# Kernel tuning notes

Measured on AMD Instinct MI355X. Metric: run time of the kernel, lower is better.

The kernel has to match this reference:

```python
import jax, jax.numpy as jnp
import numpy as np

B, N = 1, 768
C_S, C_Z, C_H, H, PQ, PV = 384, 128, 16, 12, 4, 8
INF, EPS = 1e5, 1e-8
SOFTPLUS_INV_1 = 0.541324854612918


def _quat_to_rot(q):
    # q: [..., 4] unit quaternions (w, x, y, z) -> [..., 3, 3]
    w, x, y, z = q[..., 0], q[..., 1], q[..., 2], q[..., 3]
    R = jnp.stack([
        1 - 2 * (y * y + z * z), 2 * (x * y - w * z), 2 * (x * z + w * y),
        2 * (x * y + w * z), 1 - 2 * (x * x + z * z), 2 * (y * z - w * x),
        2 * (x * z - w * y), 2 * (y * z + w * x), 1 - 2 * (x * x + y * y),
    ], axis=-1)
    return R.reshape(q.shape[:-1] + (3, 3))


def setup_inputs() -> dict:
    key = jax.random.key(0)
    ks = jax.random.split(key, 24)
    def lin(k, din, dout):
        return jax.random.normal(k, (din, dout), jnp.float32) / np.sqrt(din)
    quat = jax.random.normal(ks[2], (B, N, 4), jnp.float32)
    quat = quat / jnp.linalg.norm(quat, axis=-1, keepdims=True)
    return {
        "s": jax.random.normal(ks[0], (B, N, C_S), jnp.float32),
        "z": jax.random.normal(ks[1], (B, N, N, C_Z), jnp.float32),
        "rot": _quat_to_rot(quat),
        "trans": 10.0 * jax.random.normal(ks[3], (B, N, 3), jnp.float32),
        "mask": jnp.ones((B, N), jnp.float32),
        "wq": lin(ks[4], C_S, H * C_H), "bq": jnp.zeros((H * C_H,), jnp.float32),
        "wkv": lin(ks[5], C_S, 2 * H * C_H), "bkv": jnp.zeros((2 * H * C_H,), jnp.float32),
        "wqp": lin(ks[6], C_S, H * PQ * 3), "bqp": jnp.zeros((H * PQ * 3,), jnp.float32),
        "wkvp": lin(ks[7], C_S, H * (PQ + PV) * 3), "bkvp": jnp.zeros((H * (PQ + PV) * 3,), jnp.float32),
        "wb": lin(ks[8], C_Z, H), "bb": jnp.zeros((H,), jnp.float32),
        "wdz": lin(ks[9], C_Z, C_Z // 4), "bdz": jnp.zeros((C_Z // 4,), jnp.float32),
        "head_weights": jnp.full((H,), SOFTPLUS_INV_1, jnp.float32),
        "wout": lin(ks[10], H * (C_Z // 4 + C_H + PV * 4), C_S),
        "bout": jnp.zeros((C_S,), jnp.float32),
    }


def reference(s, z, rot, trans, mask, wq, bq, wkv, bkv, wqp, bqp, wkvp, bkvp,
              wb, bb, wdz, bdz, head_weights, wout, bout):
    # scalar q, k, v: [B, N, H, C_H]
    q = (s @ wq + bq).reshape(B, N, H, C_H)
    kv = (s @ wkv + bkv).reshape(B, N, H, 2 * C_H)
    k, v = kv[..., :C_H], kv[..., C_H:]

    def make_pts(w, b, npts):
        p = s @ w + b                                       # [B, N, H*npts*3]
        p = jnp.stack(jnp.split(p, 3, axis=-1), axis=-1)    # [B, N, H*npts, 3]
        p = jnp.einsum('bnxy,bnpy->bnpx', rot, p) + trans[:, :, None, :]
        return p.reshape(B, N, H, npts, 3)

    q_pts = make_pts(wqp, bqp, PQ)                          # [B, N, H, PQ, 3]
    kv_pts = make_pts(wkvp, bkvp, PQ + PV)
    k_pts, v_pts = kv_pts[..., :PQ, :], kv_pts[..., PQ:, :]

    b_bias = z @ wb + bb                                    # [B, N, N, H]
    a = jnp.einsum('bihc,bjhc->bhij', q, k) * np.sqrt(1.0 / (3 * C_H))
    a = a + np.sqrt(1.0 / 3) * jnp.transpose(b_bias, (0, 3, 1, 2))

    disp = q_pts[:, :, None] - k_pts[:, None]               # [B, i, j, H, PQ, 3]
    pt_att = jnp.sum(disp ** 2, axis=-1)                    # [B, i, j, H, PQ]
    hw = jax.nn.softplus(head_weights) * np.sqrt(1.0 / (3 * (PQ * 9.0 / 2)))
    pt_att = -0.5 * jnp.sum(pt_att * hw[:, None], axis=-1)  # [B, i, j, H]
    a = a + jnp.transpose(pt_att, (0, 3, 1, 2))

    sq_mask = INF * (mask[:, :, None] * mask[:, None, :] - 1.0)
    a = jax.nn.softmax(a + sq_mask[:, None], axis=-1)       # [B, H, i, j]

    o = jnp.einsum('bhij,bjhc->bihc', a, v).reshape(B, N, -1)
    o_pt = jnp.einsum('bhij,bjhpx->bihpx', a, v_pts)        # [B, N, H, PV, 3]
    o_pt = jnp.einsum('bixy,bihpx->bihpy', rot, o_pt - trans[:, :, None, None, :])
    o_pt_norm = jnp.sqrt(jnp.sum(o_pt ** 2, axis=-1) + EPS).reshape(B, N, -1)
    o_pt = o_pt.reshape(B, N, -1, 3)

    pair_z = z @ wdz + bdz                                  # [B, N, N, C_Z//4]
    o_pair = jnp.einsum('bhij,bijc->bihc', a, pair_z).reshape(B, N, -1)

    feats = jnp.concatenate(
        [o, o_pt[..., 0], o_pt[..., 1], o_pt[..., 2], o_pt_norm, o_pair], axis=-1)
    return feats @ wout + bout
```

## Files before the change

kernel.cpp:

```cpp
#include <hip/hip_runtime.h>
#include <hip/hip_bf16.h>
#include <math.h>

#define NTOK 768
#define CS   384
#define CZ   128
#define NH   12
#define INF_ 100000.0f
#define EPS_ 1e-8f

typedef unsigned int  uint32;
typedef __attribute__((ext_vector_type(8))) short bf16x8;
typedef __attribute__((ext_vector_type(4))) float f32x4;

__device__ __forceinline__ uint32 bf16rn(float x) {
    uint32 u = __float_as_uint(x);
    return (u + 0x7fffu + ((u >> 16) & 1u)) >> 16;
}
__device__ __forceinline__ float bflo(uint32 u) { return __uint_as_float((u & 0xffffu) << 16); }
__device__ __forceinline__ float bfhi(uint32 u) { return __uint_as_float(u & 0xffff0000u); }
__device__ __forceinline__ uint32 pkbf(float a, float b) {
    union { unsigned short s[2]; uint32 u; } r;
    __hip_bfloat16 ha = __float2bfloat16(a);
    __hip_bfloat16 hb = __float2bfloat16(b);
    __builtin_memcpy(&r.s[0], &ha, 2);
    __builtin_memcpy(&r.s[1], &hb, 2);
    return r.u;
}

#define QK_SCALE 0.14433756729740643f
#define B_SCALE  0.5773502691896258f
#define HW_SCALE 0.13608276348795434f

__global__ __launch_bounds__(256) void k1a_gemm(
    const float* __restrict__ s,
    const float* __restrict__ wq, const float* __restrict__ wkv,
    const float* __restrict__ wqp, const float* __restrict__ wkvp,
    float* __restrict__ RAW)
{
    __shared__ float sA[32][72];
    __shared__ float sB[32][72];
    const int tid  = threadIdx.x;
    const int tok0 = blockIdx.x * 64;
    const int col0 = blockIdx.y * 64;

    const int m0 = (tid & 15) * 4;
    const int n0 = (tid >> 4) * 4;

    float4 acc[4];
    #pragma unroll
    for (int nn = 0; nn < 4; nn++) acc[nn] = make_float4(0.f, 0.f, 0.f, 0.f);

    const int lam = tid >> 2, lak = (tid & 3) * 8;
    const int lbk = tid >> 3, lbc = (tid & 7) * 8;
    const int gcol = col0 + lbc;
    const float* wsrc; int wwidth, woff;
    if (gcol < 192)      { wsrc = wq;   wwidth = 192; woff = gcol; }
    else if (gcol < 576) { wsrc = wkv;  wwidth = 384; woff = gcol - 192; }
    else if (gcol < 720) { wsrc = wqp;  wwidth = 144; woff = gcol - 576; }
    else                 { wsrc = wkvp; wwidth = 432; woff = gcol - 720; }

    for (int kb = 0; kb < CS; kb += 32) {
        const float4 a0 = *(const float4*)&s[(tok0 + lam) * CS + kb + lak];
        const float4 a1 = *(const float4*)&s[(tok0 + lam) * CS + kb + lak + 4];
        const float4 b0 = *(const float4*)&wsrc[(size_t)(kb + lbk) * wwidth + woff];
        const float4 b1 = *(const float4*)&wsrc[(size_t)(kb + lbk) * wwidth + woff + 4];
        __syncthreads();
        sA[lak + 0][lam] = a0.x; sA[lak + 1][lam] = a0.y;
        sA[lak + 2][lam] = a0.z; sA[lak + 3][lam] = a0.w;
        sA[lak + 4][lam] = a1.x; sA[lak + 5][lam] = a1.y;
        sA[lak + 6][lam] = a1.z; sA[lak + 7][lam] = a1.w;
        *(float4*)&sB[lbk][lbc]     = b0;
        *(float4*)&sB[lbk][lbc + 4] = b1;
        __syncthreads();
        #pragma unroll
        for (int k = 0; k < 32; k++) {
            const float4 av = *(const float4*)&sA[k][m0];
            const float4 bv = *(const float4*)&sB[k][n0];
            acc[0].x += av.x * bv.x; acc[0].y += av.y * bv.x; acc[0].z += av.z * bv.x; acc[0].w += av.w * bv.x;
            acc[1].x += av.x * bv.y; acc[1].y += av.y * bv.y; acc[1].z += av.z * bv.y; acc[1].w += av.w * bv.y;
            acc[2].x += av.x * bv.z; acc[2].y += av.y * bv.z; acc[2].z += av.z * bv.z; acc[2].w += av.w * bv.z;
            acc[3].x += av.x * bv.w; acc[3].y += av.y * bv.w; acc[3].z += av.z * bv.w; acc[3].w += av.w * bv.w;
        }
    }
    #pragma unroll
    for (int nn = 0; nn < 4; nn++)
        *(float4*)&RAW[(size_t)(col0 + n0 + nn) * NTOK + tok0 + m0] = acc[nn];
}

__global__ __launch_bounds__(256) void k1b_finish(
    const float* __restrict__ RAW,
    const float* __restrict__ rot, const float* __restrict__ trans,
    const float* __restrict__ bq, const float* __restrict__ bkv,
    const float* __restrict__ bqp, const float* __restrict__ bkvp,
    const float* __restrict__ head_weights,
    float* __restrict__ VT, float* __restrict__ QP, float* __restrict__ VPT,
    float* __restrict__ AP, float* __restrict__ BP,
    float* __restrict__ RQN, float* __restrict__ CKN)
{
    __shared__ float hwS[NH];
    const int tid = threadIdx.x;
    const int t  = blockIdx.x * 16 + (tid & 15);
    const int wk = tid >> 4;

    if (tid < NH) hwS[tid] = logf(1.0f + expf(head_weights[tid])) * HW_SCALE;

    float R[9], T3[3];
    #pragma unroll
    for (int x = 0; x < 9; x++) R[x] = rot[t * 9 + x];
    #pragma unroll
    for (int x = 0; x < 3; x++) T3[x] = trans[t * 3 + x];
    __syncthreads();

    for (int col = wk; col < 192; col += 16) {
        const int h = col >> 4, c = col & 15;
        AP[(size_t)(h * 28 + c) * NTOK + t] = QK_SCALE * (RAW[(size_t)col * NTOK + t] + bq[col]);
    }
    for (int idx = wk; idx < 192; idx += 16) {
        const int h = idx >> 4, c = idx & 15;
        BP[(size_t)(h * 28 + c) * NTOK + t] = RAW[(size_t)(192 + h * 32 + c) * NTOK + t] + bkv[h * 32 + c];
        VT[idx * NTOK + t] = RAW[(size_t)(192 + h * 32 + 16 + c) * NTOK + t] + bkv[h * 32 + 16 + c];
    }
    for (int pidx = wk; pidx < 48; pidx += 16) {
        const int h = pidx >> 2, p = pidx & 3;
        const float r0 = RAW[(size_t)(576 + 0 * 48 + pidx) * NTOK + t] + bqp[0 * 48 + pidx];
        const float r1 = RAW[(size_t)(576 + 1 * 48 + pidx) * NTOK + t] + bqp[1 * 48 + pidx];
        const float r2 = RAW[(size_t)(576 + 2 * 48 + pidx) * NTOK + t] + bqp[2 * 48 + pidx];
        #pragma unroll
        for (int x = 0; x < 3; x++) {
            const float v = R[x*3+0]*r0 + R[x*3+1]*r1 + R[x*3+2]*r2 + T3[x];
            QP[t * 144 + pidx * 3 + x] = v;
            AP[(size_t)(h * 28 + 16 + p * 3 + x) * NTOK + t] = hwS[h] * v;
        }
    }
    for (int pidx = wk; pidx < 144; pidx += 16) {
        const int h = pidx / 12, pp = pidx % 12;
        const float r0 = RAW[(size_t)(720 + 0 * 144 + pidx) * NTOK + t] + bkvp[0 * 144 + pidx];
        const float r1 = RAW[(size_t)(720 + 1 * 144 + pidx) * NTOK + t] + bkvp[1 * 144 + pidx];
        const float r2 = RAW[(size_t)(720 + 2 * 144 + pidx) * NTOK + t] + bkvp[2 * 144 + pidx];
        #pragma unroll
        for (int x = 0; x < 3; x++) {
            const float v = R[x*3+0]*r0 + R[x*3+1]*r1 + R[x*3+2]*r2 + T3[x];
            if (pp < 4) BP[(size_t)(h * 28 + 16 + pp * 3 + x) * NTOK + t] = v;
            else        VPT[((h * 8 + pp - 4) * 3 + x) * NTOK + t] = v;
        }
    }
    __syncthreads();
    if (wk < NH) {
        const int h = wk;
        float sq = 0.f, sk = 0.f;
        #pragma unroll
        for (int d = 0; d < 12; d++) {
            const float a = QP[t * 144 + h * 12 + d];
            sq += a * a;
            const float b = BP[(size_t)(h * 28 + 16 + d) * NTOK + t];
            sk += b * b;
        }
        RQN[h * NTOK + t] = -0.5f * hwS[h] * sq;
        CKN[h * NTOK + t] = -0.5f * hwS[h] * sk;
    }
}

__global__ __launch_bounds__(256) void k2_zproj_mfma(
    const float* __restrict__ z, const float* __restrict__ wb, const float* __restrict__ bb,
    const float* __restrict__ wdz, const float* __restrict__ bdz,
    float* __restrict__ BBT, uint32* __restrict__ PZB)
{
    __shared__ __align__(16) unsigned short wB[48 * 136];
    __shared__ float outS[2][64][52];
    __shared__ float bbS[12], bdzS[32];

    const int tid = threadIdx.x;
    const int i   = blockIdx.x;
    const int l   = tid & 63;
    const int jt  = tid >> 6;

    for (int idx = tid; idx < 48 * 64; idx += 256) {
        const int o = idx >> 6, k2 = (idx & 63) * 2;
        float f0, f1;
        if (o < 12)      { f0 = wb[k2 * 12 + o];         f1 = wb[(k2 + 1) * 12 + o]; }
        else if (o < 44) { f0 = wdz[k2 * 32 + (o - 12)]; f1 = wdz[(k2 + 1) * 32 + (o - 12)]; }
        else             { f0 = 0.f; f1 = 0.f; }
        *(uint32*)&wB[o * 136 + k2] = pkbf(f0, f1);
    }
    if (tid < 12) bbS[tid] = bb[tid];
    else if (tid >= 32 && tid < 64) bdzS[tid - 32] = bdz[tid - 32];
    __syncthreads();

    bf16x8 Bf[3][4];
    #pragma unroll
    for (int t = 0; t < 3; t++)
        #pragma unroll
        for (int ks = 0; ks < 4; ks++)
            Bf[t][ks] = *(const bf16x8*)&wB[(t * 16 + (l & 15)) * 136 + ks * 32 + (l >> 4) * 8];

    const float* zb = z + ((size_t)i * NTOK + jt * 16 + (l & 15)) * CZ + (l >> 4) * 8;

    float4 pa[8];
    #pragma unroll
    for (int ks = 0; ks < 4; ks++) {
        pa[2 * ks]     = *(const float4*)&zb[ks * 32];
        pa[2 * ks + 1] = *(const float4*)&zb[ks * 32 + 4];
    }

    for (int tile = 0; tile < 12; tile++) {
        const int j0  = tile * 64;
        const int buf = tile & 1;

        union { uint32 u[4]; bf16x8 v; } Au[4];
        #pragma unroll
        for (int ks = 0; ks < 4; ks++) {
            Au[ks].u[0] = pkbf(pa[2 * ks].x,     pa[2 * ks].y);
            Au[ks].u[1] = pkbf(pa[2 * ks].z,     pa[2 * ks].w);
            Au[ks].u[2] = pkbf(pa[2 * ks + 1].x, pa[2 * ks + 1].y);
            Au[ks].u[3] = pkbf(pa[2 * ks + 1].z, pa[2 * ks + 1].w);
        }
        if (tile < 11) {
            const float* zn = zb + (size_t)(tile + 1) * 64 * CZ;
            #pragma unroll
            for (int ks = 0; ks < 4; ks++) {
                pa[2 * ks]     = *(const float4*)&zn[ks * 32];
                pa[2 * ks + 1] = *(const float4*)&zn[ks * 32 + 4];
            }
        }

        f32x4 acc[3];
        #pragma unroll
        for (int t = 0; t < 3; t++) acc[t] = (f32x4){0.f, 0.f, 0.f, 0.f};
        #pragma unroll
        for (int ks = 0; ks < 4; ks++)
            #pragma unroll
            for (int t = 0; t < 3; t++)
                acc[t] = __builtin_amdgcn_mfma_f32_16x16x32_bf16(Au[ks].v, Bf[t][ks], acc[t], 0, 0, 0);

        #pragma unroll
        for (int t = 0; t < 3; t++) {
            const int o = t * 16 + (l & 15);
            #pragma unroll
            for (int v = 0; v < 4; v++)
                outS[buf][jt * 16 + (l >> 4) * 4 + v][o] = acc[t][v];
        }
        __syncthreads();

        for (int idx = tid; idx < 12 * 64; idx += 256) {
            const int o = idx >> 6, jl = idx & 63;
            BBT[((size_t)i * 12 + o) * NTOK + j0 + jl] = outS[buf][jl][o] + bbS[o];
        }
        for (int idx = tid; idx < 32 * 32; idx += 256) {
            const int c = idx >> 5, jp = idx & 31;
            const float f0 = outS[buf][jp * 2][12 + c] + bdzS[c];
            const float f1 = outS[buf][jp * 2 + 1][12 + c] + bdzS[c];
            PZB[(size_t)(i * 32 + c) * 384 + (j0 >> 1) + jp] = pkbf(f0, f1);
        }
    }
}

__global__ __launch_bounds__(256) void k3a_logits(
    const float* __restrict__ AP, const float* __restrict__ BP,
    const float* __restrict__ RQN, const float* __restrict__ CKN,
    const float* __restrict__ BBT, const float* __restrict__ mask,
    float* __restrict__ LG)
{
    __shared__ float sA[28][64];
    __shared__ float sB[28][64];
    const int tid = threadIdx.x;
    const int j0 = blockIdx.x * 64;
    const int i0 = blockIdx.y * 64;
    const int h  = blockIdx.z;

    #pragma unroll
    for (int t = 0; t < 7; t++) {
        const int idx = tid + t * 256;
        const int row = idx >> 6, col = idx & 63;
        sA[row][col] = AP[(size_t)(h * 28 + row) * NTOK + i0 + col];
        sB[row][col] = BP[(size_t)(h * 28 + row) * NTOK + j0 + col];
    }
    __syncthreads();

    const int m0 = (tid & 15) * 4;
    const int n0 = (tid >> 4) * 4;

    float4 acc[4];
    #pragma unroll
    for (int mm = 0; mm < 4; mm++) acc[mm] = make_float4(0.f, 0.f, 0.f, 0.f);

    #pragma unroll
    for (int k = 0; k < 28; k++) {
        const float4 av = *(const float4*)&sA[k][m0];
        const float4 bv = *(const float4*)&sB[k][n0];
        acc[0].x += av.x * bv.x; acc[0].y += av.x * bv.y; acc[0].z += av.x * bv.z; acc[0].w += av.x * bv.w;
        acc[1].x += av.y * bv.x; acc[1].y += av.y * bv.y; acc[1].z += av.y * bv.z; acc[1].w += av.y * bv.w;
        acc[2].x += av.z * bv.x; acc[2].y += av.z * bv.y; acc[2].z += av.z * bv.z; acc[2].w += av.z * bv.w;
        acc[3].x += av.w * bv.x; acc[3].y += av.w * bv.y; acc[3].z += av.w * bv.z; acc[3].w += av.w * bv.w;
    }

    const float4 ck = *(const float4*)&CKN[h * NTOK + j0 + n0];
    const float4 mj = *(const float4*)&mask[j0 + n0];
    #pragma unroll
    for (int mm = 0; mm < 4; mm++) {
        const int gi = i0 + m0 + mm;
        const float rq = RQN[h * NTOK + gi];
        const float mi = mask[gi];
        const float4 bb = *(const float4*)&BBT[((size_t)gi * NH + h) * NTOK + j0 + n0];
        float4 o;
        o.x = acc[mm].x + B_SCALE * bb.x + rq + ck.x + INF_ * (mi * mj.x - 1.0f);
        o.y = acc[mm].y + B_SCALE * bb.y + rq + ck.y + INF_ * (mi * mj.y - 1.0f);
        o.z = acc[mm].z + B_SCALE * bb.z + rq + ck.z + INF_ * (mi * mj.z - 1.0f);
        o.w = acc[mm].w + B_SCALE * bb.w + rq + ck.w + INF_ * (mi * mj.w - 1.0f);
        *(float4*)&LG[((size_t)gi * NH + h) * NTOK + j0 + n0] = o;
    }
}

__global__ __launch_bounds__(768) void k3b_attn(
    const float* __restrict__ LG,
    const float* __restrict__ VT, const float* __restrict__ VPT,
    const uint32* __restrict__ PZB,
    float* __restrict__ O, float* __restrict__ OPT, float* __restrict__ OPAIR)
{
    __shared__ float LB[NH][NTOK];
    const int i = blockIdx.x, tid = threadIdx.x;

    #pragma unroll
    for (int hh = 0; hh < NH; hh++)
        LB[hh][tid] = LG[((size_t)i * NH + hh) * NTOK + tid];
    __syncthreads();

    const int h = tid >> 6, l = tid & 63;

    {
        float m = -3.0e38f;
        for (int jj = l; jj < NTOK; jj += 64) m = fmaxf(m, LB[h][jj]);
        #pragma unroll
        for (int off = 32; off >= 1; off >>= 1) m = fmaxf(m, __shfl_xor(m, off));
        float ssum = 0.0f;
        for (int jj = l; jj < NTOK; jj += 64) {
            const float e = __expf(LB[h][jj] - m);
            LB[h][jj] = e;
            ssum += e;
        }
        #pragma unroll
        for (int off = 32; off >= 1; off >>= 1) ssum += __shfl_xor(ssum, off);
        const float inv = 1.0f / ssum;
        for (int jj = l; jj < NTOK; jj += 64) LB[h][jj] *= inv;
    }
    __syncthreads();

    #pragma unroll 2
    for (int r = 0; r < 40; r++) {
        const float4* src = (r < 16) ? (const float4*)&VT[(h * 16 + r) * NTOK]
                                     : (const float4*)&VPT[(h * 24 + (r - 16)) * NTOK];
        const float4 v0 = src[l],       p0 = *(const float4*)&LB[h][l * 4];
        const float4 v1 = src[64 + l],  p1 = *(const float4*)&LB[h][256 + l * 4];
        const float4 v2 = src[128 + l], p2 = *(const float4*)&LB[h][512 + l * 4];
        float acc = p0.x*v0.x + p0.y*v0.y + p0.z*v0.z + p0.w*v0.w
                  + p1.x*v1.x + p1.y*v1.y + p1.z*v1.z + p1.w*v1.w
                  + p2.x*v2.x + p2.y*v2.y + p2.z*v2.z + p2.w*v2.w;
        #pragma unroll
        for (int off = 32; off >= 1; off >>= 1) acc += __shfl_xor(acc, off);
        if (l == 0) {
            if (r < 16) O[i * 192 + h * 16 + r] = acc;
            else        OPT[i * 288 + h * 24 + (r - 16)] = acc;
        }
    }
    #pragma unroll 2
    for (int c = 0; c < 32; c++) {
        const uint2* src = (const uint2*)PZB + (size_t)(i * 32 + c) * 192;
        float a = 0.f;
        #pragma unroll
        for (int it = 0; it < 3; it++) {
            const uint2 u = src[it * 64 + l];
            const float4 p = *(const float4*)&LB[h][it * 256 + l * 4];
            a += p.x * bflo(u.x) + p.y * bfhi(u.x)
               + p.z * bflo(u.y) + p.w * bfhi(u.y);
        }
        #pragma unroll
        for (int off = 32; off >= 1; off >>= 1) a += __shfl_xor(a, off);
        if (l == 0) OPAIR[i * 384 + h * 32 + c] = a;
    }
}

#define K4T 8
__global__ __launch_bounds__(256) void k4_out(
    const float* __restrict__ O, const float* __restrict__ OPT, const float* __restrict__ OPAIR,
    const float* __restrict__ rot, const float* __restrict__ trans,
    const float* __restrict__ wout, const float* __restrict__ bout,
    float* __restrict__ out)
{
    __shared__ float f[K4T][960];
    const int n0 = blockIdx.x * K4T, tid = threadIdx.x;

    for (int idx = tid; idx < K4T * 192; idx += 256) {
        const int t = idx / 192, k = idx % 192;
        f[t][k] = O[(n0 + t) * 192 + k];
    }
    for (int idx = tid; idx < K4T * 384; idx += 256) {
        const int t = idx / 384, k = idx % 384;
        f[t][576 + k] = OPAIR[(n0 + t) * 384 + k];
    }
    for (int idx = tid; idx < K4T * 96; idx += 256) {
        const int t = idx / 96, hp = idx % 96;
        const int n = n0 + t;
        const float vx = OPT[n * 288 + hp * 3 + 0] - trans[n * 3 + 0];
        const float vy = OPT[n * 288 + hp * 3 + 1] - trans[n * 3 + 1];
        const float vz = OPT[n * 288 + hp * 3 + 2] - trans[n * 3 + 2];
        const float o0 = rot[n*9+0]*vx + rot[n*9+3]*vy + rot[n*9+6]*vz;
        const float o1 = rot[n*9+1]*vx + rot[n*9+4]*vy + rot[n*9+7]*vz;
        const float o2 = rot[n*9+2]*vx + rot[n*9+5]*vy + rot[n*9+8]*vz;
        f[t][192 + hp] = o0;
        f[t][288 + hp] = o1;
        f[t][384 + hp] = o2;
        f[t][480 + hp] = sqrtf(o0*o0 + o1*o1 + o2*o2 + EPS_);
    }
    __syncthreads();

    for (int o = tid; o < 384; o += 256) {
        float acc[K4T];
        #pragma unroll
        for (int t = 0; t < K4T; t++) acc[t] = bout[o];
        for (int kq = 0; kq < 240; kq++) {
            float4 fv[K4T];
            #pragma unroll
            for (int t = 0; t < K4T; t++) fv[t] = *(const float4*)&f[t][kq * 4];
            #pragma unroll
            for (int kk = 0; kk < 4; kk++) {
                const float wv = wout[(kq * 4 + kk) * 384 + o];
                #pragma unroll
                for (int t = 0; t < K4T; t++) {
                    const float fe = (kk == 0) ? fv[t].x : (kk == 1) ? fv[t].y
                                   : (kk == 2) ? fv[t].z : fv[t].w;
                    acc[t] += fe * wv;
                }
            }
        }
        #pragma unroll
        for (int t = 0; t < K4T; t++) out[(n0 + t) * 384 + o] = acc[t];
    }
}

extern "C" void kernel_launch(void* const* d_in, const int* in_sizes, int n_in,
                              void* d_out, int out_size, void* d_ws, size_t ws_size,
                              hipStream_t stream) {
    (void)in_sizes; (void)n_in; (void)out_size; (void)ws_size;
    const float* s     = (const float*)d_in[0];
    const float* z     = (const float*)d_in[1];
    const float* rot   = (const float*)d_in[2];
    const float* trans = (const float*)d_in[3];
    const float* mask  = (const float*)d_in[4];
    const float* wq    = (const float*)d_in[5];
    const float* bq    = (const float*)d_in[6];
    const float* wkv   = (const float*)d_in[7];
    const float* bkv   = (const float*)d_in[8];
    const float* wqp   = (const float*)d_in[9];
    const float* bqp   = (const float*)d_in[10];
    const float* wkvp  = (const float*)d_in[11];
    const float* bkvp  = (const float*)d_in[12];
    const float* wb    = (const float*)d_in[13];
    const float* bb    = (const float*)d_in[14];
    const float* wdz   = (const float*)d_in[15];
    const float* bdz   = (const float*)d_in[16];
    const float* hwts  = (const float*)d_in[17];
    const float* wout  = (const float*)d_in[18];
    const float* bout  = (const float*)d_in[19];
    float* out = (float*)d_out;

    float* ws = (float*)d_ws;
    float* Q     = ws;
    float* KT    = Q     + 147456;
    float* VT    = KT    + 147456;
    float* QP    = VT    + 147456;
    float* KPT   = QP    + 110592;
    float* VPT   = KPT   + 110592;
    float* O     = VPT   + 221184;
    float* OPT   = O     + 147456;
    float* OPAIR = OPT   + 221184;
    float* BBT   = OPAIR + 294912;
    uint32* PZB  = (uint32*)(BBT + 7077888);
    float* AP    = BBT + 7077888 + 9437184;
    float* BP    = AP  + 258048;
    float* RQN   = BP  + 258048;
    float* CKN   = RQN + 9216;
    float* LG    = CKN + 9216;
    float* RAW = BBT;

    hipLaunchKernelGGL(k1a_gemm, dim3(NTOK / 64, 1152 / 64), dim3(256), 0, stream,
                       s, wq, wkv, wqp, wkvp, RAW);
    hipLaunchKernelGGL(k1b_finish, dim3(NTOK / 16), dim3(256), 0, stream,
                       RAW, rot, trans, bq, bkv, bqp, bkvp, hwts,
                       VT, QP, VPT, AP, BP, RQN, CKN);
    hipLaunchKernelGGL(k2_zproj_mfma, dim3(NTOK), dim3(256), 0, stream,
                       z, wb, bb, wdz, bdz, BBT, PZB);
    hipLaunchKernelGGL(k3a_logits, dim3(NTOK / 64, NTOK / 64, NH), dim3(256), 0, stream,
                       AP, BP, RQN, CKN, BBT, mask, LG);
    hipLaunchKernelGGL(k3b_attn, dim3(NTOK), dim3(768), 0, stream,
                       LG, VT, VPT, PZB, O, OPT, OPAIR);
    hipLaunchKernelGGL(k4_out, dim3(NTOK / K4T), dim3(256), 0, stream,
                       O, OPT, OPAIR, rot, trans, wout, bout, out);
}
```

Baseline: 391.4 us.

## Fuse logits computation with softmax and attention, keeping probabilities in registers

Merges the separate logits kernel and attention kernel into one kernel per query row. Each wavefront computes its head's logits directly from the point-projection factors, keeps the softmax probabilities in registers, and drops the LG intermediate buffer and its global round trip. The BP factors are now read from global memory per row rather than reused through a shared-memory tile, so those reads grow and rely on caching. A shared-memory padding tweak in the z-projection kernel is also included to reduce bank conflicts.

```diff
diff --git a/kernel.cpp b/kernel.cpp
--- a/kernel.cpp
+++ b/kernel.cpp
@@ -13,10 +13,6 @@
 typedef __attribute__((ext_vector_type(8))) short bf16x8;
 typedef __attribute__((ext_vector_type(4))) float f32x4;
 
-__device__ __forceinline__ uint32 bf16rn(float x) {
-    uint32 u = __float_as_uint(x);
-    return (u + 0x7fffu + ((u >> 16) & 1u)) >> 16;
-}
 __device__ __forceinline__ float bflo(uint32 u) { return __uint_as_float((u & 0xffffu) << 16); }
 __device__ __forceinline__ float bfhi(uint32 u) { return __uint_as_float(u & 0xffff0000u); }
 __device__ __forceinline__ uint32 pkbf(float a, float b) {
@@ -167,7 +163,7 @@
     float* __restrict__ BBT, uint32* __restrict__ PZB)
 {
     __shared__ __align__(16) unsigned short wB[48 * 136];
-    __shared__ float outS[2][64][52];
+    __shared__ float outS[2][64][53];
     __shared__ float bbS[12], bdzS[32];
 
     const int tid = threadIdx.x;
@@ -255,106 +251,76 @@
     }
 }
 
-__global__ __launch_bounds__(256) void k3a_logits(
+__global__ __launch_bounds__(768) void k3_fused(
     const float* __restrict__ AP, const float* __restrict__ BP,
     const float* __restrict__ RQN, const float* __restrict__ CKN,
     const float* __restrict__ BBT, const float* __restrict__ mask,
-    float* __restrict__ LG)
-{
-    __shared__ float sA[28][64];
-    __shared__ float sB[28][64];
-    const int tid = threadIdx.x;
-    const int j0 = blockIdx.x * 64;
-    const int i0 = blockIdx.y * 64;
-    const int h  = blockIdx.z;
-
-    #pragma unroll
-    for (int t = 0; t < 7; t++) {
-        const int idx = tid + t * 256;
-        const int row = idx >> 6, col = idx & 63;
-        sA[row][col] = AP[(size_t)(h * 28 + row) * NTOK + i0 + col];
-        sB[row][col] = BP[(size_t)(h * 28 + row) * NTOK + j0 + col];
-    }
-    __syncthreads();
-
-    const int m0 = (tid & 15) * 4;
-    const int n0 = (tid >> 4) * 4;
-
-    float4 acc[4];
-    #pragma unroll
-    for (int mm = 0; mm < 4; mm++) acc[mm] = make_float4(0.f, 0.f, 0.f, 0.f);
-
-    #pragma unroll
-    for (int k = 0; k < 28; k++) {
-        const float4 av = *(const float4*)&sA[k][m0];
-        const float4 bv = *(const float4*)&sB[k][n0];
-        acc[0].x += av.x * bv.x; acc[0].y += av.x * bv.y; acc[0].z += av.x * bv.z; acc[0].w += av.x * bv.w;
-        acc[1].x += av.y * bv.x; acc[1].y += av.y * bv.y; acc[1].z += av.y * bv.z; acc[1].w += av.y * bv.w;
-        acc[2].x += av.z * bv.x; acc[2].y += av.z * bv.y; acc[2].z += av.z * bv.z; acc[2].w += av.z * bv.w;
-        acc[3].x += av.w * bv.x; acc[3].y += av.w * bv.y; acc[3].z += av.w * bv.z; acc[3].w += av.w * bv.w;
-    }
-
-    const float4 ck = *(const float4*)&CKN[h * NTOK + j0 + n0];
-    const float4 mj = *(const float4*)&mask[j0 + n0];
-    #pragma unroll
-    for (int mm = 0; mm < 4; mm++) {
-        const int gi = i0 + m0 + mm;
-        const float rq = RQN[h * NTOK + gi];
-        const float mi = mask[gi];
-        const float4 bb = *(const float4*)&BBT[((size_t)gi * NH + h) * NTOK + j0 + n0];
-        float4 o;
-        o.x = acc[mm].x + B_SCALE * bb.x + rq + ck.x + INF_ * (mi * mj.x - 1.0f);
-        o.y = acc[mm].y + B_SCALE * bb.y + rq + ck.y + INF_ * (mi * mj.y - 1.0f);
-        o.z = acc[mm].z + B_SCALE * bb.z + rq + ck.z + INF_ * (mi * mj.z - 1.0f);
-        o.w = acc[mm].w + B_SCALE * bb.w + rq + ck.w + INF_ * (mi * mj.w - 1.0f);
-        *(float4*)&LG[((size_t)gi * NH + h) * NTOK + j0 + n0] = o;
-    }
-}
-
-__global__ __launch_bounds__(768) void k3b_attn(
-    const float* __restrict__ LG,
     const float* __restrict__ VT, const float* __restrict__ VPT,
     const uint32* __restrict__ PZB,
     float* __restrict__ O, float* __restrict__ OPT, float* __restrict__ OPAIR)
 {
-    __shared__ float LB[NH][NTOK];
     const int i = blockIdx.x, tid = threadIdx.x;
-
-    #pragma unroll
-    for (int hh = 0; hh < NH; hh++)
-        LB[hh][tid] = LG[((size_t)i * NH + hh) * NTOK + tid];
-    __syncthreads();
-
     const int h = tid >> 6, l = tid & 63;
 
-    {
-        float m = -3.0e38f;
-        for (int jj = l; jj < NTOK; jj += 64) m = fmaxf(m, LB[h][jj]);
-        #pragma unroll
-        for (int off = 32; off >= 1; off >>= 1) m = fmaxf(m, __shfl_xor(m, off));
-        float ssum = 0.0f;
-        for (int jj = l; jj < NTOK; jj += 64) {
-            const float e = __expf(LB[h][jj] - m);
-            LB[h][jj] = e;
+    float ap[28];
+    #pragma unroll
+    for (int k = 0; k < 28; k++) ap[k] = AP[(size_t)(h * 28 + k) * NTOK + i];
+    const float rq = RQN[h * NTOK + i];
+    const float mi = mask[i];
+
+    f32x4 lg[3];
+    #pragma unroll
+    for (int qb = 0; qb < 3; qb++) {
+        const int j4 = qb * 256 + l * 4;
+        const float4 ck  = *(const float4*)&CKN[h * NTOK + j4];
+        const float4 bbv = *(const float4*)&BBT[((size_t)i * 12 + h) * NTOK + j4];
+        const float4 mj  = *(const float4*)&mask[j4];
+        f32x4 a;
+        a[0] = B_SCALE * bbv.x + rq + ck.x + INF_ * (mi * mj.x - 1.0f);
+        a[1] = B_SCALE * bbv.y + rq + ck.y + INF_ * (mi * mj.y - 1.0f);
+        a[2] = B_SCALE * bbv.z + rq + ck.z + INF_ * (mi * mj.z - 1.0f);
+        a[3] = B_SCALE * bbv.w + rq + ck.w + INF_ * (mi * mj.w - 1.0f);
+        #pragma unroll
+        for (int k = 0; k < 28; k++) {
+            const float4 bp = *(const float4*)&BP[(size_t)(h * 28 + k) * NTOK + j4];
+            a[0] += ap[k] * bp.x; a[1] += ap[k] * bp.y;
+            a[2] += ap[k] * bp.z; a[3] += ap[k] * bp.w;
+        }
+        lg[qb] = a;
+    }
+
+    float m = -3.0e38f;
+    #pragma unroll
+    for (int qb = 0; qb < 3; qb++)
+        #pragma unroll
+        for (int v = 0; v < 4; v++) m = fmaxf(m, lg[qb][v]);
+    #pragma unroll
+    for (int off = 32; off >= 1; off >>= 1) m = fmaxf(m, __shfl_xor(m, off));
+    float ssum = 0.0f;
+    #pragma unroll
+    for (int qb = 0; qb < 3; qb++)
+        #pragma unroll
+        for (int v = 0; v < 4; v++) {
+            const float e = __expf(lg[qb][v] - m);
+            lg[qb][v] = e;
             ssum += e;
         }
-        #pragma unroll
-        for (int off = 32; off >= 1; off >>= 1) ssum += __shfl_xor(ssum, off);
-        const float inv = 1.0f / ssum;
-        for (int jj = l; jj < NTOK; jj += 64) LB[h][jj] *= inv;
-    }
-    __syncthreads();
+    #pragma unroll
+    for (int off = 32; off >= 1; off >>= 1) ssum += __shfl_xor(ssum, off);
+    const float inv = 1.0f / ssum;
+    #pragma unroll
+    for (int qb = 0; qb < 3; qb++)
+        #pragma unroll
+        for (int v = 0; v < 4; v++) lg[qb][v] *= inv;
 
     #pragma unroll 2
     for (int r = 0; r < 40; r++) {
         const float4* src = (r < 16) ? (const float4*)&VT[(h * 16 + r) * NTOK]
                                      : (const float4*)&VPT[(h * 24 + (r - 16)) * NTOK];
-        const float4 v0 = src[l],       p0 = *(const float4*)&LB[h][l * 4];
-        const float4 v1 = src[64 + l],  p1 = *(const float4*)&LB[h][256 + l * 4];
-        const float4 v2 = src[128 + l], p2 = *(const float4*)&LB[h][512 + l * 4];
-        float acc = p0.x*v0.x + p0.y*v0.y + p0.z*v0.z + p0.w*v0.w
-                  + p1.x*v1.x + p1.y*v1.y + p1.z*v1.z + p1.w*v1.w
-                  + p2.x*v2.x + p2.y*v2.y + p2.z*v2.z + p2.w*v2.w;
+        const float4 v0 = src[l], v1 = src[64 + l], v2 = src[128 + l];
+        float acc = lg[0][0]*v0.x + lg[0][1]*v0.y + lg[0][2]*v0.z + lg[0][3]*v0.w
+                  + lg[1][0]*v1.x + lg[1][1]*v1.y + lg[1][2]*v1.z + lg[1][3]*v1.w
+                  + lg[2][0]*v2.x + lg[2][1]*v2.y + lg[2][2]*v2.z + lg[2][3]*v2.w;
         #pragma unroll
         for (int off = 32; off >= 1; off >>= 1) acc += __shfl_xor(acc, off);
         if (l == 0) {
@@ -369,9 +335,8 @@
         #pragma unroll
         for (int it = 0; it < 3; it++) {
             const uint2 u = src[it * 64 + l];
-            const float4 p = *(const float4*)&LB[h][it * 256 + l * 4];
-            a += p.x * bflo(u.x) + p.y * bfhi(u.x)
-               + p.z * bflo(u.y) + p.w * bfhi(u.y);
+            a += lg[it][0] * bflo(u.x) + lg[it][1] * bfhi(u.x)
+               + lg[it][2] * bflo(u.y) + lg[it][3] * bfhi(u.y);
         }
         #pragma unroll
         for (int off = 32; off >= 1; off >>= 1) a += __shfl_xor(a, off);
@@ -479,7 +444,6 @@
     float* BP    = AP  + 258048;
     float* RQN   = BP  + 258048;
     float* CKN   = RQN + 9216;
-    float* LG    = CKN + 9216;
     float* RAW = BBT;
 
     hipLaunchKernelGGL(k1a_gemm, dim3(NTOK / 64, 1152 / 64), dim3(256), 0, stream,
@@ -489,10 +453,9 @@
                        VT, QP, VPT, AP, BP, RQN, CKN);
     hipLaunchKernelGGL(k2_zproj_mfma, dim3(NTOK), dim3(256), 0, stream,
                        z, wb, bb, wdz, bdz, BBT, PZB);
-    hipLaunchKernelGGL(k3a_logits, dim3(NTOK / 64, NTOK / 64, NH), dim3(256), 0, stream,
-                       AP, BP, RQN, CKN, BBT, mask, LG);
-    hipLaunchKernelGGL(k3b_attn, dim3(NTOK), dim3(768), 0, stream,
-                       LG, VT, VPT, PZB, O, OPT, OPAIR);
+    hipLaunchKernelGGL(k3_fused, dim3(NTOK), dim3(768), 0, stream,
+                       AP, BP, RQN, CKN, BBT, mask, VT, VPT, PZB,
+                       O, OPT, OPAIR);
     hipLaunchKernelGGL(k4_out, dim3(NTOK / K4T), dim3(256), 0, stream,
                        O, OPT, OPAIR, rot, trans, wout, bout, out);
 }
```

Result: no change. 383.9 us (-1.9%).
